# Kernel tuning notes

Hardware: AMD Instinct MI355X
Metric: run time of the kernel (lower is better)

The kernel has to match this reference:

```python
import jax, jax.numpy as jnp
import numpy as np

HIDDEN = 768
BATCH = 128


def setup_inputs() -> dict:
    key = jax.random.key(0)
    k_in, k_op = jax.random.split(key)
    inputs = jax.random.normal(k_in, (BATCH, HIDDEN, HIDDEN), dtype=jnp.float32)
    # nn.init.uniform_(operator, 0, 1)
    operator = jax.random.uniform(k_op, (HIDDEN, HIDDEN), dtype=jnp.float32)
    return {"inputs": inputs, "operator": operator}


def reference(inputs, operator):
    # Original: diag(operator @ inputs @ operator^T) then softmax over dim axis.
    # diag_i = sum_{j,k} operator[i,j] * inputs[b,j,k] * operator[i,k]
    # Compute first GEMM, then fuse the second matmul's diagonal as a dot-reduction.
    mm = jnp.einsum('ij,bjk->bik', operator, inputs)      # [b, d, d]
    diag = jnp.einsum('bik,ik->bi', mm, operator)          # [b, d]
    return jax.nn.softmax(diag, axis=1)
```

## Files before the change

kernel.cpp:

```cpp
#include <hip/hip_runtime.h>

#define HID 768
#define NB  128

using short8  = __attribute__((ext_vector_type(8))) short;
using short4_t = __attribute__((ext_vector_type(4))) short;
using float4_t = __attribute__((ext_vector_type(4))) float;

__device__ __forceinline__ short f2bf(float x) {
    union { float f; unsigned u; } c; c.f = x;
    unsigned r = c.u + 0x7fffu + ((c.u >> 16) & 1u);
    return (short)(r >> 16);
}
__device__ __forceinline__ float bf2f(short b) {
    union { unsigned u; float f; } c; c.u = ((unsigned)(unsigned short)b) << 16;
    return c.f;
}

__global__ __launch_bounds__(256, 3)
void diag_quad_kernel(const float* __restrict__ X, const float* __restrict__ OP,
                      float* __restrict__ out)
{
    constexpr int LDT = 40;
    __shared__ __align__(16) short Ah_s[128 * LDT];
    __shared__ __align__(16) short Al_s[128 * LDT];
    __shared__ __align__(16) short Bh_s[128 * LDT];
    __shared__ __align__(16) short Bl_s[128 * LDT];
    __shared__ float Dred[2][128];

    const int tid  = threadIdx.x;
    const int b    = blockIdx.x / 6;
    const int it   = blockIdx.x % 6;
    const int i0   = it * 128;
    const float* Xb = X + (size_t)b * HID * HID;

    const int lane = tid & 63;
    const int wave = tid >> 6;
    const int wj = wave & 1;
    const int wi = wave >> 1;
    const int m16 = lane & 15;
    const int kg  = lane >> 4;

    const int srow = tid >> 3;
    const int scol = (tid & 7) * 4;

    float p[4] = {0.f, 0.f, 0.f, 0.f};

    for (int jt = 0; jt < 6; ++jt) {
        const int j0 = jt * 128;
        float4_t acc[4][4];
#pragma unroll
        for (int a = 0; a < 4; ++a)
#pragma unroll
            for (int c = 0; c < 4; ++c) acc[a][c] = (float4_t){0.f, 0.f, 0.f, 0.f};

        for (int ks = 0; ks < 24; ++ks) {
            const int k0 = ks * 32;
            __syncthreads();
#pragma unroll
            for (int pp = 0; pp < 4; ++pp) {
                const int row = pp * 32 + srow;
                const float4_t xv = *(const float4_t*)(Xb + (size_t)(j0 + row) * HID + k0 + scol);
                const float4_t ov = *(const float4_t*)(OP + (size_t)(i0 + row) * HID + k0 + scol);
                short4_t xh, xl, oh, ol;
#pragma unroll
                for (int e = 0; e < 4; ++e) {
                    const short hb = f2bf(xv[e]); xh[e] = hb; xl[e] = f2bf(xv[e] - bf2f(hb));
                    const short ob = f2bf(ov[e]); oh[e] = ob; ol[e] = f2bf(ov[e] - bf2f(ob));
                }
                *(short4_t*)(&Ah_s[row * LDT + scol]) = xh;
                *(short4_t*)(&Al_s[row * LDT + scol]) = xl;
                *(short4_t*)(&Bh_s[row * LDT + scol]) = oh;
                *(short4_t*)(&Bl_s[row * LDT + scol]) = ol;
            }
            __syncthreads();

            short8 fah[4], fal[4], fbh[4], fbl[4];
#pragma unroll
            for (int ti = 0; ti < 4; ++ti) {
                const int row = wj * 64 + ti * 16 + m16;
                fah[ti] = *(const short8*)(&Ah_s[row * LDT + kg * 8]);
                fal[ti] = *(const short8*)(&Al_s[row * LDT + kg * 8]);
            }
#pragma unroll
            for (int tj = 0; tj < 4; ++tj) {
                const int row = wi * 64 + tj * 16 + m16;
                fbh[tj] = *(const short8*)(&Bh_s[row * LDT + kg * 8]);
                fbl[tj] = *(const short8*)(&Bl_s[row * LDT + kg * 8]);
            }
#pragma unroll
            for (int ti = 0; ti < 4; ++ti)
#pragma unroll
                for (int tj = 0; tj < 4; ++tj) {
                    acc[ti][tj] = __builtin_amdgcn_mfma_f32_16x16x32_bf16(fah[ti], fbh[tj], acc[ti][tj], 0, 0, 0);
                    acc[ti][tj] = __builtin_amdgcn_mfma_f32_16x16x32_bf16(fal[ti], fbh[tj], acc[ti][tj], 0, 0, 0);
                    acc[ti][tj] = __builtin_amdgcn_mfma_f32_16x16x32_bf16(fah[ti], fbl[tj], acc[ti][tj], 0, 0, 0);
                }
        }

#pragma unroll
        for (int tj = 0; tj < 4; ++tj) {
            const int i_abs = i0 + wi * 64 + tj * 16 + m16;
            float s = 0.f;
#pragma unroll
            for (int ti = 0; ti < 4; ++ti) {
                const int j_base = j0 + wj * 64 + ti * 16 + kg * 4;
                const float4_t opv = *(const float4_t*)(OP + (size_t)i_abs * HID + j_base);
#pragma unroll
                for (int r = 0; r < 4; ++r) s += acc[ti][tj][r] * opv[r];
            }
            p[tj] += s;
        }
    }

#pragma unroll
    for (int tj = 0; tj < 4; ++tj) {
        p[tj] += __shfl_xor(p[tj], 16);
        p[tj] += __shfl_xor(p[tj], 32);
    }
    if (kg == 0) {
#pragma unroll
        for (int tj = 0; tj < 4; ++tj)
            Dred[wj][wi * 64 + tj * 16 + m16] = p[tj];
    }
    __syncthreads();
    if (tid < 128)
        out[(size_t)b * HID + i0 + tid] = Dred[0][tid] + Dred[1][tid];
}

__global__ __launch_bounds__(768)
void softmax_rows(float* __restrict__ out)
{
    const int row = blockIdx.x;
    const int t = threadIdx.x;
    const int wave = t >> 6, lane = t & 63;
    __shared__ float redm[12];
    __shared__ float reds[12];

    float v = out[(size_t)row * HID + t];

    float m = v;
#pragma unroll
    for (int o = 32; o >= 1; o >>= 1) m = fmaxf(m, __shfl_xor(m, o));
    if (lane == 0) redm[wave] = m;
    __syncthreads();
    if (t == 0) {
        float mm = redm[0];
        for (int w = 1; w < 12; ++w) mm = fmaxf(mm, redm[w]);
        redm[0] = mm;
    }
    __syncthreads();
    m = redm[0];

    const float e = expf(v - m);
    float s = e;
#pragma unroll
    for (int o = 32; o >= 1; o >>= 1) s += __shfl_xor(s, o);
    if (lane == 0) reds[wave] = s;
    __syncthreads();
    if (t == 0) {
        float ss = 0.f;
        for (int w = 0; w < 12; ++w) ss += reds[w];
        reds[0] = ss;
    }
    __syncthreads();
    out[(size_t)row * HID + t] = e / reds[0];
}

extern "C" void kernel_launch(void* const* d_in, const int* in_sizes, int n_in,
                              void* d_out, int out_size, void* d_ws, size_t ws_size,
                              hipStream_t stream)
{
    const float* X  = (const float*)d_in[0];
    const float* OP = (const float*)d_in[1];
    float* out = (float*)d_out;

    hipLaunchKernelGGL(diag_quad_kernel, dim3(NB * 6), dim3(256), 0, stream, X, OP, out);
    hipLaunchKernelGGL(softmax_rows, dim3(NB), dim3(768), 0, stream, out);
}
```

Baseline: 723.8 us.

## Pre-split operator into fp16 fragment layout and widen X tile per block

```diff
diff --git a/kernel.cpp b/kernel.cpp
--- a/kernel.cpp
+++ b/kernel.cpp
@@ -3,54 +3,71 @@
 #define HID 768
 #define NB  128
 
-using short8  = __attribute__((ext_vector_type(8))) short;
-using short4_t = __attribute__((ext_vector_type(4))) short;
-using float4_t = __attribute__((ext_vector_type(4))) float;
+typedef _Float16 half8  __attribute__((ext_vector_type(8)));
+typedef _Float16 half4v __attribute__((ext_vector_type(4)));
+typedef float    float4_t __attribute__((ext_vector_type(4)));
 
-__device__ __forceinline__ short f2bf(float x) {
-    union { float f; unsigned u; } c; c.f = x;
-    unsigned r = c.u + 0x7fffu + ((c.u >> 16) & 1u);
-    return (short)(r >> 16);
-}
-__device__ __forceinline__ float bf2f(short b) {
-    union { unsigned u; float f; } c; c.u = ((unsigned)(unsigned short)b) << 16;
-    return c.f;
+#define OP_TILES (48 * 24)
+#define OP_PLANE ((size_t)OP_TILES * 64 * 8)
+
+__global__ __launch_bounds__(256)
+void split_op(const float* __restrict__ OP, _Float16* __restrict__ ws)
+{
+    const int g    = blockIdx.x * 256 + threadIdx.x;
+    const int tile = g >> 6, lane = g & 63;
+    const int it16 = tile / 24, ks = tile % 24;
+    const int i = it16 * 16 + (lane & 15);
+    const int k = ks * 32 + (lane >> 4) * 8;
+    const float4_t a = *(const float4_t*)(OP + (size_t)i * HID + k);
+    const float4_t b = *(const float4_t*)(OP + (size_t)i * HID + k + 4);
+    half8 h, l;
+#pragma unroll
+    for (int e = 0; e < 4; ++e) {
+        _Float16 h0 = (_Float16)a[e]; h[e]     = h0; l[e]     = (_Float16)(a[e] - (float)h0);
+        _Float16 h1 = (_Float16)b[e]; h[e + 4] = h1; l[e + 4] = (_Float16)(b[e] - (float)h1);
+    }
+    *(half8*)(ws + (size_t)(tile * 64 + lane) * 8) = h;
+    *(half8*)(ws + OP_PLANE + (size_t)(tile * 64 + lane) * 8) = l;
 }
 
-__global__ __launch_bounds__(256, 3)
+__global__ __launch_bounds__(256, 2)
 void diag_quad_kernel(const float* __restrict__ X, const float* __restrict__ OP,
-                      float* __restrict__ out)
+                      const _Float16* __restrict__ opws, float* __restrict__ out)
 {
-    constexpr int LDT = 40;
-    __shared__ __align__(16) short Ah_s[128 * LDT];
-    __shared__ __align__(16) short Al_s[128 * LDT];
-    __shared__ __align__(16) short Bh_s[128 * LDT];
-    __shared__ __align__(16) short Bl_s[128 * LDT];
+    __shared__ __align__(16) _Float16 Ah[256 * 32];
+    __shared__ __align__(16) _Float16 Al[256 * 32];
     __shared__ float Dred[2][128];
 
-    const int tid  = threadIdx.x;
-    const int b    = blockIdx.x / 6;
-    const int it   = blockIdx.x % 6;
+    const int idx  = blockIdx.x;
+    const int xcd  = idx & 7, slot = idx >> 3;
+    const int b    = xcd * 16 + slot / 6;
+    const int it   = slot % 6;
     const int i0   = it * 128;
     const float* Xb = X + (size_t)b * HID * HID;
 
+    const int tid  = threadIdx.x;
     const int lane = tid & 63;
     const int wave = tid >> 6;
-    const int wj = wave & 1;
-    const int wi = wave >> 1;
-    const int m16 = lane & 15;
-    const int kg  = lane >> 4;
+    const int wj   = wave & 1;
+    const int wi   = wave >> 1;
+    const int m16  = lane & 15;
+    const int kg   = lane >> 4;
 
     const int srow = tid >> 3;
     const int scol = (tid & 7) * 4;
+    const int kgw  = scol >> 3;
+    const int off4 = scol & 7;
+
+    const int fragbase = (kg * 16 + m16) * 8;
+    const int it16base = it * 8 + wi * 4;
 
     float p[4] = {0.f, 0.f, 0.f, 0.f};
 
-    for (int jt = 0; jt < 6; ++jt) {
-        const int j0 = jt * 128;
-        float4_t acc[4][4];
+    for (int jt = 0; jt < 3; ++jt) {
+        const int j0 = jt * 256;
+        float4_t acc[8][4];
 #pragma unroll
-        for (int a = 0; a < 4; ++a)
+        for (int a = 0; a < 8; ++a)
 #pragma unroll
             for (int c = 0; c < 4; ++c) acc[a][c] = (float4_t){0.f, 0.f, 0.f, 0.f};
 
@@ -58,44 +75,41 @@
             const int k0 = ks * 32;
             __syncthreads();
 #pragma unroll
-            for (int pp = 0; pp < 4; ++pp) {
-                const int row = pp * 32 + srow;
-                const float4_t xv = *(const float4_t*)(Xb + (size_t)(j0 + row) * HID + k0 + scol);
-                const float4_t ov = *(const float4_t*)(OP + (size_t)(i0 + row) * HID + k0 + scol);
-                short4_t xh, xl, oh, ol;
+            for (int pp = 0; pp < 8; ++pp) {
+                const int r = pp * 32 + srow;
+                const float4_t v = *(const float4_t*)(Xb + (size_t)(j0 + r) * HID + k0 + scol);
+                half4v hv, lv;
 #pragma unroll
                 for (int e = 0; e < 4; ++e) {
-                    const short hb = f2bf(xv[e]); xh[e] = hb; xl[e] = f2bf(xv[e] - bf2f(hb));
-                    const short ob = f2bf(ov[e]); oh[e] = ob; ol[e] = f2bf(ov[e] - bf2f(ob));
+                    _Float16 hh = (_Float16)v[e];
+                    hv[e] = hh; lv[e] = (_Float16)(v[e] - (float)hh);
                 }
-                *(short4_t*)(&Ah_s[row * LDT + scol]) = xh;
-                *(short4_t*)(&Al_s[row * LDT + scol]) = xl;
-                *(short4_t*)(&Bh_s[row * LDT + scol]) = oh;
-                *(short4_t*)(&Bl_s[row * LDT + scol]) = ol;
+                const int ca = ((r >> 4) * 64 + kgw * 16 + (r & 15)) * 8 + off4;
+                *(half4v*)&Ah[ca] = hv;
+                *(half4v*)&Al[ca] = lv;
+            }
+
+            half8 bh[4], bl[4];
+            const size_t obase = ((size_t)it16base * 24 + ks) * 512 + (size_t)lane * 8;
+#pragma unroll
+            for (int tj = 0; tj < 4; ++tj) {
+                bh[tj] = *(const half8*)(opws + obase + (size_t)tj * 24 * 512);
+                bl[tj] = *(const half8*)(opws + OP_PLANE + obase + (size_t)tj * 24 * 512);
             }
             __syncthreads();
 
-            short8 fah[4], fal[4], fbh[4], fbl[4];
 #pragma unroll
-            for (int ti = 0; ti < 4; ++ti) {
-                const int row = wj * 64 + ti * 16 + m16;
-                fah[ti] = *(const short8*)(&Ah_s[row * LDT + kg * 8]);
-                fal[ti] = *(const short8*)(&Al_s[row * LDT + kg * 8]);
-            }
-#pragma unroll
-            for (int tj = 0; tj < 4; ++tj) {
-                const int row = wi * 64 + tj * 16 + m16;
-                fbh[tj] = *(const short8*)(&Bh_s[row * LDT + kg * 8]);
-                fbl[tj] = *(const short8*)(&Bl_s[row * LDT + kg * 8]);
-            }
-#pragma unroll
-            for (int ti = 0; ti < 4; ++ti)
+            for (int ti = 0; ti < 8; ++ti) {
+                const int rt = wj * 8 + ti;
+                const half8 ah = *(const half8*)&Ah[rt * 512 + fragbase];
+                const half8 al = *(const half8*)&Al[rt * 512 + fragbase];
 #pragma unroll
                 for (int tj = 0; tj < 4; ++tj) {
-                    acc[ti][tj] = __builtin_amdgcn_mfma_f32_16x16x32_bf16(fah[ti], fbh[tj], acc[ti][tj], 0, 0, 0);
-                    acc[ti][tj] = __builtin_amdgcn_mfma_f32_16x16x32_bf16(fal[ti], fbh[tj], acc[ti][tj], 0, 0, 0);
-                    acc[ti][tj] = __builtin_amdgcn_mfma_f32_16x16x32_bf16(fah[ti], fbl[tj], acc[ti][tj], 0, 0, 0);
+                    acc[ti][tj] = __builtin_amdgcn_mfma_f32_16x16x32_f16(ah, bh[tj], acc[ti][tj], 0, 0, 0);
+                    acc[ti][tj] = __builtin_amdgcn_mfma_f32_16x16x32_f16(al, bh[tj], acc[ti][tj], 0, 0, 0);
+                    acc[ti][tj] = __builtin_amdgcn_mfma_f32_16x16x32_f16(ah, bl[tj], acc[ti][tj], 0, 0, 0);
                 }
+            }
         }
 
 #pragma unroll
@@ -103,11 +117,11 @@
             const int i_abs = i0 + wi * 64 + tj * 16 + m16;
             float s = 0.f;
 #pragma unroll
-            for (int ti = 0; ti < 4; ++ti) {
-                const int j_base = j0 + wj * 64 + ti * 16 + kg * 4;
-                const float4_t opv = *(const float4_t*)(OP + (size_t)i_abs * HID + j_base);
+            for (int ti = 0; ti < 8; ++ti) {
+                const int jb = j0 + wj * 128 + ti * 16 + kg * 4;
+                const float4_t ov = *(const float4_t*)(OP + (size_t)i_abs * HID + jb);
 #pragma unroll
-                for (int r = 0; r < 4; ++r) s += acc[ti][tj][r] * opv[r];
+                for (int r = 0; r < 4; ++r) s += acc[ti][tj][r] * ov[r];
             }
             p[tj] += s;
         }
@@ -174,7 +188,9 @@
     const float* X  = (const float*)d_in[0];
     const float* OP = (const float*)d_in[1];
     float* out = (float*)d_out;
+    _Float16* opws = (_Float16*)d_ws;
 
-    hipLaunchKernelGGL(diag_quad_kernel, dim3(NB * 6), dim3(256), 0, stream, X, OP, out);
+    hipLaunchKernelGGL(split_op, dim3(OP_TILES / 4), dim3(256), 0, stream, OP, opws);
+    hipLaunchKernelGGL(diag_quad_kernel, dim3(NB * 6), dim3(256), 0, stream, X, OP, opws, out);
     hipLaunchKernelGGL(softmax_rows, dim3(NB), dim3(768), 0, stream, out);
 }
```

After: 1.120 ms. 1.55x slower.
